# Optimization experiments

Hardware: AMD Instinct MI355X
Metric: run time of the kernel (lower is better)

## Reference

```python
import jax, jax.numpy as jnp
import numpy as np

HEADS, HEAD_DIM, NQP, NVP = 12, 16, 4, 8
NODE_DIM, EDGE_DIM = 384, 128
B, N = 1, 768


def setup_inputs() -> dict:
    key = jax.random.key(0)
    ks = jax.random.split(key, 12)
    node_features = jax.random.normal(ks[0], (B, N, NODE_DIM), dtype=jnp.float32)
    edge_features = jax.random.normal(ks[1], (B, N, N, EDGE_DIM), dtype=jnp.float32)
    # random valid rotations via QR of gaussian matrices (well-conditioned for inverse)
    A = jax.random.normal(ks[2], (B, N, 3, 3), dtype=jnp.float32)
    Q, _ = jnp.linalg.qr(A)
    R = Q
    t = jax.random.normal(ks[3], (B, N, 3), dtype=jnp.float32)
    def lin(k, din, dout):
        return jax.random.normal(k, (din, dout), dtype=jnp.float32) / np.sqrt(din)
    Wqkv = lin(ks[4], NODE_DIM, 3 * HEADS * HEAD_DIM)
    Wvqk = lin(ks[5], NODE_DIM, 2 * 3 * NQP * HEADS)
    Wvv = lin(ks[6], NODE_DIM, 3 * NVP * HEADS)
    Webias = lin(ks[7], EDGE_DIM, HEADS)
    fin_in = HEADS * EDGE_DIM + HEADS * HEAD_DIM + HEADS * NVP * 4
    Wfin = lin(ks[8], fin_in, NODE_DIM)
    bfin = jnp.zeros((NODE_DIM,), dtype=jnp.float32)
    return {"node_features": node_features, "edge_features": edge_features,
            "R": R, "t": t, "Wqkv": Wqkv, "Wvqk": Wvqk, "Wvv": Wvv,
            "Webias": Webias, "Wfin": Wfin, "bfin": bfin}


def _ipa(node_features, edge_features, R, t, Wqkv, Wvqk, Wvv, Webias, Wfin, bfin):
    b, n, _ = node_features.shape
    h, d, p, pv = HEADS, HEAD_DIM, NQP, NVP
    # scalar q, k, v: [b, h, n, d]
    qkv = (node_features @ Wqkv).reshape(b, n, 3, h, d)
    sq, sk, sv = [jnp.transpose(qkv[:, :, i], (0, 2, 1, 3)) for i in range(3)]
    node_scalar = jnp.einsum('bhid,bhjd->bhij', sq, sk) * (d ** -0.5)
    edge_bias = jnp.einsum('bijd,dh->bhij', edge_features, Webias)
    # vector q/k in local frames: [b, h, n, p, 3]
    vqk = (node_features @ Wvqk).reshape(b, n, 2, h, p, 3)
    vq = jnp.transpose(vqk[:, :, 0], (0, 2, 1, 3, 4))
    vk = jnp.transpose(vqk[:, :, 1], (0, 2, 1, 3, 4))
    t_e = t[:, None, :, None, :]  # [b,1,n,1,3]
    gq = jnp.einsum('bnij,bhnpj->bhnpi', R, vq) + t_e
    gk = jnp.einsum('bnij,bhnpj->bhnpi', R, vk) + t_e
    # ||gk_i - gq_j||^2 summed over (p,3), expanded to avoid [b,h,n,n,p,3]
    wc = np.sqrt(2.0 / 9.0 / p) / 2.0
    k_sq = jnp.sum(gk * gk, axis=(-1, -2))  # [b,h,n]
    q_sq = jnp.sum(gq * gq, axis=(-1, -2))  # [b,h,n]
    cross = jnp.einsum('bhipd,bhjpd->bhij', gk, gq)
    dist = (k_sq[:, :, :, None] + q_sq[:, :, None, :] - 2.0 * cross) * wc
    attn = jax.nn.softmax((node_scalar + edge_bias - dist) * (3 ** -0.5), axis=-1)
    # aggregations
    edge_out = jnp.einsum('bhij,bijd->bihd', attn, edge_features)     # [b,n,h,edge_dim]
    scalar_out = jnp.einsum('bhij,bhjd->bihd', attn, sv)              # [b,n,h,d]
    vv = (node_features @ Wvv).reshape(b, n, h, pv, 3)
    vv = jnp.transpose(vv, (0, 2, 1, 3, 4))                            # [b,h,n,pv,3]
    gvv = jnp.einsum('bnij,bhnpj->bhnpi', R, vv) + t_e
    att_v = jnp.einsum('bhij,bhjpd->bihpd', attn, gvv)                # [b,n,h,pv,3]
    Rinv = jnp.linalg.inv(R)
    local_v = jnp.einsum('bnij,bnhpj->bnhpi', Rinv, att_v - t[:, :, None, None, :])
    v_len = jnp.sqrt(jnp.sum(local_v * local_v, axis=-1))             # [b,n,h,pv]
    combined = jnp.concatenate([
        edge_out.reshape(b, n, -1),
        scalar_out.reshape(b, n, -1),
        local_v.reshape(b, n, -1),
        v_len.reshape(b, n, -1),
    ], axis=-1)
    return node_features + combined @ Wfin + bfin


def reference(node_features, edge_features, R, t, Wqkv, Wvqk, Wvv, Webias, Wfin, bfin):
    return _ipa(node_features, edge_features, R, t, Wqkv, Wvqk, Wvv, Webias, Wfin, bfin)
```

## Files before the change

### kernel.cpp

```cpp
#include <hip/hip_runtime.h>
#include <cmath>


namespace {

constexpr int NN = 768;
constexpr int NH = 12;

constexpr float S3 = 0.5773502691896258f;
constexpr float C1 = 0.25f * S3;
constexpr float C2 = 0.23570226039551584f * S3;
constexpr float C3 = 0.11785113019775792f * S3;

typedef float f32x4 __attribute__((ext_vector_type(4)));
typedef short bf16x8 __attribute__((ext_vector_type(8)));
typedef unsigned int u32x4 __attribute__((ext_vector_type(4)));
typedef unsigned int u32x2 __attribute__((ext_vector_type(2)));
typedef _Float16 f16x2 __attribute__((ext_vector_type(2)));

#define LGKM0 asm volatile("s_waitcnt lgkmcnt(0)" ::: "memory")
#define SCHED0 __builtin_amdgcn_sched_barrier(0)

__device__ inline unsigned cvt_pk_bf16(float lo, float hi) {
  unsigned r;
  asm volatile("v_cvt_pk_bf16_f32 %0, %1, %2" : "=v"(r) : "v"(lo), "v"(hi));
  return r;
}

__device__ inline float fdot2(unsigned a, unsigned b, float c) {
#if __has_builtin(__builtin_amdgcn_fdot2)
  return __builtin_amdgcn_fdot2(__builtin_bit_cast(f16x2, a),
                                __builtin_bit_cast(f16x2, b), c, false);
#else
  union U { unsigned u; _Float16 h[2]; } x, y;
  x.u = a; y.u = b;
  return c + (float)x.h[0] * (float)y.h[0] + (float)x.h[1] * (float)y.h[1];
#endif
}

__device__ inline u32x2 tr_read(unsigned addr) {
  u32x2 d;
  asm volatile("ds_read_b64_tr_b16 %0, %1" : "=v"(d) : "v"(addr));
  return d;
}

__device__ inline f32x4 mfma16(u32x2 a, u32x2 b, f32x4 c) {
  asm volatile("v_mfma_f32_16x16x16_bf16 %0, %1, %2, %0"
               : "+v"(c) : "v"(a), "v"(b));
  return c;
}

__device__ inline unsigned pkf16(float a, float b) {
  union U { _Float16 h[2]; unsigned u; } x;
  x.h[0] = (_Float16)a; x.h[1] = (_Float16)b;
  return x.u;
}

__global__ __launch_bounds__(288) void k_proj(const float* __restrict__ node,
    const float* __restrict__ Wqkv, const float* __restrict__ Wvqk,
    const float* __restrict__ Wvv, float* __restrict__ proj) {
  __shared__ __align__(16) float nl[2][384];
  const int i0 = blockIdx.x * 2;
  const int tid = threadIdx.x;
  for (int idx = tid; idx < 2 * 384; idx += 288)
    ((float*)nl)[idx] = node[(size_t)i0 * 384 + idx];
  __syncthreads();
  const int c0 = tid * 4;
  const float* W; int ld, col;
  if (c0 < 576)      { W = Wqkv; ld = 576; col = c0; }
  else if (c0 < 864) { W = Wvqk; ld = 288; col = c0 - 576; }
  else               { W = Wvv;  ld = 288; col = c0 - 864; }
  float4 acc[2];
#pragma unroll
  for (int r = 0; r < 2; ++r) acc[r] = make_float4(0.f, 0.f, 0.f, 0.f);
#pragma unroll 4
  for (int k = 0; k < 384; ++k) {
    const float4 w4 = *(const float4*)&W[(size_t)k * ld + col];
#pragma unroll
    for (int r = 0; r < 2; ++r) {
      const float nv = nl[r][k];
      acc[r].x += nv * w4.x; acc[r].y += nv * w4.y;
      acc[r].z += nv * w4.z; acc[r].w += nv * w4.w;
    }
  }
#pragma unroll
  for (int r = 0; r < 2; ++r)
    *(float4*)&proj[(size_t)(i0 + r) * 1152 + c0] = acc[r];
}

__global__ __launch_bounds__(256) void k_geom(const float* __restrict__ proj,
    const float* __restrict__ R, const float* __restrict__ t,
    unsigned* __restrict__ Bph, unsigned* __restrict__ Sgh,
    float* __restrict__ V) {
  const int gid = blockIdx.x * 256 + threadIdx.x;
  if (gid >= NN * NH) return;
  const int n = gid / NH, h = gid % NH;
  const float* pr = proj + (size_t)n * 1152;
  const float* Rn = R + n * 9;
  const float t0 = t[n * 3 + 0], t1 = t[n * 3 + 1], t2 = t[n * 3 + 2];
  const size_t hn = (size_t)h * NN + n;
  unsigned* bp = Bph + ((size_t)n * NH + h) * 16;
  unsigned* sg = Sgh + ((size_t)n * NH + h) * 16;
#pragma unroll
  for (int m = 0; m < 8; ++m) {
    bp[m] = pkf16(C1 * pr[(12 + h) * 16 + 2 * m], C1 * pr[(12 + h) * 16 + 2 * m + 1]);
    sg[m] = pkf16(pr[h * 16 + 2 * m], pr[h * 16 + 2 * m + 1]);
    V[hn * 40 + 2 * m]     = pr[(24 + h) * 16 + 2 * m];
    V[hn * 40 + 2 * m + 1] = pr[(24 + h) * 16 + 2 * m + 1];
  }
  float gq[12], gk[12];
  float qs = 0.f, ks = 0.f;
#pragma unroll
  for (int p = 0; p < 4; ++p) {
    {
      const float vx = pr[576 + (h * 4 + p) * 3 + 0];
      const float vy = pr[576 + (h * 4 + p) * 3 + 1];
      const float vz = pr[576 + (h * 4 + p) * 3 + 2];
      const float g0 = Rn[0] * vx + Rn[1] * vy + Rn[2] * vz + t0;
      const float g1 = Rn[3] * vx + Rn[4] * vy + Rn[5] * vz + t1;
      const float g2 = Rn[6] * vx + Rn[7] * vy + Rn[8] * vz + t2;
      gq[p * 3 + 0] = g0; gq[p * 3 + 1] = g1; gq[p * 3 + 2] = g2;
      qs += g0 * g0 + g1 * g1 + g2 * g2;
    }
    {
      const float vx = pr[576 + ((12 + h) * 4 + p) * 3 + 0];
      const float vy = pr[576 + ((12 + h) * 4 + p) * 3 + 1];
      const float vz = pr[576 + ((12 + h) * 4 + p) * 3 + 2];
      const float g0 = Rn[0] * vx + Rn[1] * vy + Rn[2] * vz + t0;
      const float g1 = Rn[3] * vx + Rn[4] * vy + Rn[5] * vz + t1;
      const float g2 = Rn[6] * vx + Rn[7] * vy + Rn[8] * vz + t2;
      gk[p * 3 + 0] = g0; gk[p * 3 + 1] = g1; gk[p * 3 + 2] = g2;
      ks += g0 * g0 + g1 * g1 + g2 * g2;
    }
  }
#pragma unroll
  for (int m = 0; m < 6; ++m) {
    bp[8 + m] = pkf16(C2 * gq[2 * m], C2 * gq[2 * m + 1]);
    sg[8 + m] = pkf16(gk[2 * m], gk[2 * m + 1]);
  }
  bp[14] = pkf16(-C3 * qs, 1.0f);
  sg[14] = pkf16(1.0f, -C3 * ks);
  bp[15] = 0u; sg[15] = 0u;
#pragma unroll
  for (int p = 0; p < 8; ++p) {
    const float vx = pr[864 + (h * 8 + p) * 3 + 0];
    const float vy = pr[864 + (h * 8 + p) * 3 + 1];
    const float vz = pr[864 + (h * 8 + p) * 3 + 2];
    V[hn * 40 + 16 + p * 3 + 0] = Rn[0] * vx + Rn[1] * vy + Rn[2] * vz + t0;
    V[hn * 40 + 16 + p * 3 + 1] = Rn[3] * vx + Rn[4] * vy + Rn[5] * vz + t1;
    V[hn * 40 + 16 + p * 3 + 2] = Rn[6] * vx + Rn[7] * vy + Rn[8] * vz + t2;
  }
}

__global__ __launch_bounds__(256, 3) void k_fused(
    const float* __restrict__ edge, const float* __restrict__ Webias,
    const unsigned* __restrict__ Bph, const unsigned* __restrict__ Sgh,
    unsigned* __restrict__ pTu, float* __restrict__ m_t,
    float* __restrict__ eout, float* __restrict__ msm,
    float* __restrict__ linv) {
  __shared__ __align__(16) unsigned short etS[4][2112];
  __shared__ __align__(16) float Osh[4][8][16][16];
  __shared__ float msh[4][16];
  __shared__ float lsh[4][16];
  const int i = blockIdx.x;
  const int tid = threadIdx.x;
  const int lane = tid & 63;
  const int w = __builtin_amdgcn_readfirstlane(tid >> 6);
  const int g = lane >> 4;
  const int c16 = lane & 15;
  const int hc = c16 < 12 ? c16 : 11;

  const unsigned etbase =
      (unsigned)(uintptr_t)(__attribute__((address_space(3))) unsigned short*)&etS[w][0];

  bf16x8 wbfrag[4];
#pragma unroll
  for (int kk = 0; kk < 4; ++kk) {
    union Pk { unsigned u[4]; bf16x8 v; } pk;
#pragma unroll
    for (int e2 = 0; e2 < 4; ++e2) {
      const int d = kk * 32 + g * 8 + 2 * e2;
      const float lo = (c16 < 12) ? S3 * Webias[d * 12 + c16] : 0.f;
      const float hi = (c16 < 12) ? S3 * Webias[(d + 1) * 12 + c16] : 0.f;
      pk.u[e2] = cvt_pk_bf16(lo, hi);
    }
    wbfrag[kk] = pk.v;
  }

  const unsigned* sgp = Sgh + ((size_t)i * NH + hc) * 16;
  const u32x4 sg0 = *(const u32x4*)(sgp + 0);
  const u32x4 sg1 = *(const u32x4*)(sgp + 4);
  const u32x4 sg2 = *(const u32x4*)(sgp + 8);
  const u32x4 sg3 = *(const u32x4*)(sgp + 12);

  float m = -3.0e38f;
  float lsum = 0.f;
  f32x4 acc[8];
#pragma unroll
  for (int dt = 0; dt < 8; ++dt) acc[dt] = (f32x4){0.f, 0.f, 0.f, 0.f};

  float4 ra[8];
  auto load8 = [&](int t) {
    const int jw = t * 64 + w * 16;
#pragma unroll
    for (int q = 0; q < 4; ++q) {
      const int f8 = lane + 64 * q;
      const int j = f8 >> 4, c8 = f8 & 15;
      const float* gp = &edge[((size_t)(i * NN + jw + j)) * 128 + c8 * 8];
      ra[2 * q]     = *(const float4*)gp;
      ra[2 * q + 1] = *(const float4*)(gp + 4);
    }
  };
  auto store8 = [&]() {
#pragma unroll
    for (int q = 0; q < 4; ++q) {
      const int f8 = lane + 64 * q;
      const int j = f8 >> 4, c8 = f8 & 15;
      u32x4 pk;
      pk.x = cvt_pk_bf16(ra[2 * q].x,     ra[2 * q].y);
      pk.y = cvt_pk_bf16(ra[2 * q].z,     ra[2 * q].w);
      pk.z = cvt_pk_bf16(ra[2 * q + 1].x, ra[2 * q + 1].y);
      pk.w = cvt_pk_bf16(ra[2 * q + 1].z, ra[2 * q + 1].w);
      *(u32x4*)&etS[w][(c8 >> 1) * 264 + j * 16 + 8 * (c8 & 1)] = pk;
    }
  };

  load8(0);

#pragma unroll 1
  for (int t = 0; t < 12; ++t) {
    const int tw = t * 4 + w;
    LGKM0;
    store8();
    SCHED0;
    if (t < 11) load8(t + 1);

    f32x4 ebacc = {0.f, 0.f, 0.f, 0.f};
#pragma unroll
    for (int kk = 0; kk < 4; ++kk) {
      const int dt = 2 * kk + (g >> 1);
      const bf16x8 a = *(const bf16x8*)&etS[w][dt * 264 + c16 * 16 + 8 * (g & 1)];
      ebacc = __builtin_amdgcn_mfma_f32_16x16x32_bf16(a, wbfrag[kk], ebacc, 0, 0, 0);
    }

    float lg[4];
#pragma unroll
    for (int r = 0; r < 4; ++r) {
      const unsigned* bpp = Bph + ((size_t)(tw * 16 + 4 * g + r) * NH + hc) * 16;
      const u32x4 b0 = *(const u32x4*)(bpp + 0);
      const u32x4 b1 = *(const u32x4*)(bpp + 4);
      const u32x4 b2 = *(const u32x4*)(bpp + 8);
      const u32x4 b3 = *(const u32x4*)(bpp + 12);
      float a = ebacc[r];
      a = fdot2(b0.x, sg0.x, a); a = fdot2(b0.y, sg0.y, a);
      a = fdot2(b0.z, sg0.z, a); a = fdot2(b0.w, sg0.w, a);
      a = fdot2(b1.x, sg1.x, a); a = fdot2(b1.y, sg1.y, a);
      a = fdot2(b1.z, sg1.z, a); a = fdot2(b1.w, sg1.w, a);
      a = fdot2(b2.x, sg2.x, a); a = fdot2(b2.y, sg2.y, a);
      a = fdot2(b2.z, sg2.z, a); a = fdot2(b2.w, sg2.w, a);
      a = fdot2(b3.x, sg3.x, a); a = fdot2(b3.y, sg3.y, a);
      a = fdot2(b3.z, sg3.z, a);
      lg[r] = a;
    }

    const float lmax = fmaxf(fmaxf(lg[0], lg[1]), fmaxf(lg[2], lg[3]));
    if (__any(lmax > m + 6.f)) {
      float tm = lmax;
      tm = fmaxf(tm, __shfl_xor(tm, 16, 64));
      tm = fmaxf(tm, __shfl_xor(tm, 32, 64));
      const float mn = fmaxf(m, tm);
      const float f = __expf(m - mn);
      m = mn;
      lsum *= f;
      float fr[4];
#pragma unroll
      for (int r = 0; r < 4; ++r) fr[r] = __shfl(f, 4 * g + r, 64);
#pragma unroll
      for (int dt = 0; dt < 8; ++dt) {
        acc[dt][0] *= fr[0]; acc[dt][1] *= fr[1];
        acc[dt][2] *= fr[2]; acc[dt][3] *= fr[3];
      }
    }
    float p0 = __expf(lg[0] - m), p1 = __expf(lg[1] - m);
    float p2 = __expf(lg[2] - m), p3 = __expf(lg[3] - m);
    lsum += (p0 + p1) + (p2 + p3);
    const unsigned pk0 = cvt_pk_bf16(p0, p1);
    const unsigned pk1 = cvt_pk_bf16(p2, p3);
    pTu[((size_t)i * 48 + tw) * 128 + g * 16 + c16]      = pk0;
    pTu[((size_t)i * 48 + tw) * 128 + 64 + g * 16 + c16] = pk1;
    if (g == 0) m_t[((size_t)i * 48 + tw) * 16 + c16] = m;

    u32x2 bfr[8];
#pragma unroll
    for (int dt = 0; dt < 8; ++dt) {
      const unsigned addr = etbase + (unsigned)(dt * 528 + g * 128 + c16 * 8);
      bfr[dt] = tr_read(addr);
    }
    LGKM0; SCHED0;
    u32x2 apk; apk.x = pk0; apk.y = pk1;
#pragma unroll
    for (int dt = 0; dt < 8; ++dt) acc[dt] = mfma16(apk, bfr[dt], acc[dt]);
  }

#pragma unroll
  for (int dt = 0; dt < 8; ++dt)
#pragma unroll
    for (int r = 0; r < 4; ++r)
      Osh[w][dt][c16][4 * g + r] = acc[dt][r];
  float ls = lsum;
  ls += __shfl_xor(ls, 16, 64);
  ls += __shfl_xor(ls, 32, 64);
  if (lane < 16) { msh[w][lane] = m; lsh[w][lane] = ls; }
  __syncthreads();
  for (int idx = tid; idx < 12 * 128; idx += 256) {
    const int h = idx >> 7, d = idx & 127;
    const int dt = d >> 4, dp = d & 15;
    const float m0 = msh[0][h], m1 = msh[1][h], m2 = msh[2][h], m3 = msh[3][h];
    const float mb = fmaxf(fmaxf(m0, m1), fmaxf(m2, m3));
    const float f0 = __expf(m0 - mb), f1 = __expf(m1 - mb);
    const float f2 = __expf(m2 - mb), f3 = __expf(m3 - mb);
    const float lb = lsh[0][h] * f0 + lsh[1][h] * f1 + lsh[2][h] * f2 + lsh[3][h] * f3;
    const float O = Osh[0][dt][dp][h] * f0 + Osh[1][dt][dp][h] * f1
                  + Osh[2][dt][dp][h] * f2 + Osh[3][dt][dp][h] * f3;
    eout[(size_t)i * 1536 + h * 128 + d] = O / lb;
    if (d == 0) {
      msm[(size_t)h * NN + i] = mb;
      linv[(size_t)h * NN + i] = 1.0f / lb;
    }
  }
}

__global__ __launch_bounds__(320) void k_scav(const unsigned* __restrict__ pTu,
    const float* __restrict__ m_t, const float* __restrict__ msm,
    const float* __restrict__ linv, const float* __restrict__ V,
    float* __restrict__ scav) {
  __shared__ __align__(16) float At[64][20];
  __shared__ __align__(16) float Vt[64][40];
  __shared__ __align__(16) float red[320 * 8];
  const int i0 = blockIdx.x * 16;
  const int h  = blockIdx.y;
  const int tid = threadIdx.x;
  const int js = tid / 80, rem = tid % 80;
  const int rg = rem / 20, cp = rem % 20;
  float2 a0 = {0.f, 0.f}, a1 = {0.f, 0.f}, a2 = {0.f, 0.f}, a3 = {0.f, 0.f};
  for (int jt = 0; jt < 12; ++jt) {
    __syncthreads();
    for (int idx = tid; idx < 1024; idx += 320) {
      const int r = idx >> 6, jj = idx & 63;
      const int i = i0 + r;
      const int tw = jt * 4 + (jj >> 4);
      const int gg = (jj & 15) >> 2, e = jj & 3;
      const unsigned u = pTu[((size_t)i * 48 + tw) * 128 + (e >> 1) * 64 + gg * 16 + h];
      const float p = __uint_as_float((e & 1) ? (u & 0xffff0000u) : (u << 16));
      const float fac = __expf(m_t[((size_t)i * 48 + tw) * 16 + h] - msm[(size_t)h * NN + i])
                      * linv[(size_t)h * NN + i];
      At[jj][r] = p * fac;
    }
    for (int idx = tid; idx < 2560; idx += 320) {
      const int jj = idx / 40, c = idx % 40;
      Vt[jj][c] = V[((size_t)h * NN + jt * 64 + jj) * 40 + c];
    }
    __syncthreads();
#pragma unroll 4
    for (int s = 0; s < 16; ++s) {
      const int jj = js * 16 + s;
      const float4 a4 = *(const float4*)&At[jj][rg * 4];
      const float2 b2 = *(const float2*)&Vt[jj][cp * 2];
      a0.x += a4.x * b2.x; a0.y += a4.x * b2.y;
      a1.x += a4.y * b2.x; a1.y += a4.y * b2.y;
      a2.x += a4.z * b2.x; a2.y += a4.z * b2.y;
      a3.x += a4.w * b2.x; a3.y += a4.w * b2.y;
    }
  }
  __syncthreads();
  *(float4*)&red[tid * 8 + 0] = make_float4(a0.x, a0.y, a1.x, a1.y);
  *(float4*)&red[tid * 8 + 4] = make_float4(a2.x, a2.y, a3.x, a3.y);
  __syncthreads();
  if (tid < 80) {
    const int rg2 = tid / 20, cp2 = tid % 20;
    float4 s0 = make_float4(0.f, 0.f, 0.f, 0.f), s1 = s0;
#pragma unroll
    for (int q = 0; q < 4; ++q) {
      const float4 r0 = *(const float4*)&red[(tid + q * 80) * 8 + 0];
      const float4 r1 = *(const float4*)&red[(tid + q * 80) * 8 + 4];
      s0.x += r0.x; s0.y += r0.y; s0.z += r0.z; s0.w += r0.w;
      s1.x += r1.x; s1.y += r1.y; s1.z += r1.z; s1.w += r1.w;
    }
    const size_t base = (size_t)h * NN + i0 + rg2 * 4;
    *(float2*)&scav[(base + 0) * 40 + cp2 * 2] = make_float2(s0.x, s0.y);
    *(float2*)&scav[(base + 1) * 40 + cp2 * 2] = make_float2(s0.z, s0.w);
    *(float2*)&scav[(base + 2) * 40 + cp2 * 2] = make_float2(s1.x, s1.y);
    *(float2*)&scav[(base + 3) * 40 + cp2 * 2] = make_float2(s1.z, s1.w);
  }
}

__global__ __launch_bounds__(256) void k_comb(
    const float* __restrict__ R, const float* __restrict__ t,
    const float* __restrict__ eout, const float* __restrict__ scav,
    float* __restrict__ comb) {
  const int i0 = blockIdx.x * 4;
  const int tid = threadIdx.x;
  __shared__ float rinv[4][9];
  __shared__ float tl[4][3];
  if (tid < 4) {
    const int i = i0 + tid;
    const float* Rn = R + i * 9;
    const float r00 = Rn[0], r01 = Rn[1], r02 = Rn[2];
    const float r10 = Rn[3], r11 = Rn[4], r12 = Rn[5];
    const float r20 = Rn[6], r21 = Rn[7], r22 = Rn[8];
    const float det = r00 * (r11 * r22 - r12 * r21)
                    - r01 * (r10 * r22 - r12 * r20)
                    + r02 * (r10 * r21 - r11 * r20);
    const float id = 1.0f / det;
    rinv[tid][0] = (r11 * r22 - r12 * r21) * id;
    rinv[tid][1] = (r02 * r21 - r01 * r22) * id;
    rinv[tid][2] = (r01 * r12 - r02 * r11) * id;
    rinv[tid][3] = (r12 * r20 - r10 * r22) * id;
    rinv[tid][4] = (r00 * r22 - r02 * r20) * id;
    rinv[tid][5] = (r02 * r10 - r00 * r12) * id;
    rinv[tid][6] = (r10 * r21 - r11 * r20) * id;
    rinv[tid][7] = (r01 * r20 - r00 * r21) * id;
    rinv[tid][8] = (r00 * r11 - r01 * r10) * id;
    tl[tid][0] = t[i * 3 + 0]; tl[tid][1] = t[i * 3 + 1]; tl[tid][2] = t[i * 3 + 2];
  }
  __syncthreads();
  for (int idx = tid; idx < 4 * 2112; idx += 256) {
    const int r = idx / 2112, k = idx % 2112;
    const int i = i0 + r;
    float val;
    if (k < 1536) {
      val = eout[(size_t)i * 1536 + k];
    } else if (k < 1728) {
      const int s = k - 1536, h = s >> 4, d = s & 15;
      val = scav[((size_t)h * NN + i) * 40 + d];
    } else if (k < 2016) {
      const int s = k - 1728, h = s / 24, rem = s % 24, p = rem / 3, x = rem % 3;
      const float* av = scav + ((size_t)h * NN + i) * 40 + 16 + p * 3;
      const float a0 = av[0] - tl[r][0], a1 = av[1] - tl[r][1], a2 = av[2] - tl[r][2];
      val = rinv[r][x * 3 + 0] * a0 + rinv[r][x * 3 + 1] * a1 + rinv[r][x * 3 + 2] * a2;
    } else {
      const int s = k - 2016, h = s >> 3, p = s & 7;
      const float* av = scav + ((size_t)h * NN + i) * 40 + 16 + p * 3;
      const float a0 = av[0] - tl[r][0], a1 = av[1] - tl[r][1], a2 = av[2] - tl[r][2];
      const float l0 = rinv[r][0] * a0 + rinv[r][1] * a1 + rinv[r][2] * a2;
      const float l1 = rinv[r][3] * a0 + rinv[r][4] * a1 + rinv[r][5] * a2;
      const float l2 = rinv[r][6] * a0 + rinv[r][7] * a1 + rinv[r][8] * a2;
      val = sqrtf(l0 * l0 + l1 * l1 + l2 * l2);
    }
    comb[(size_t)i * 2112 + k] = val;
  }
}

__global__ __launch_bounds__(256) void k_finalA(
    const float* __restrict__ comb, const float* __restrict__ Wfin,
    float* __restrict__ partial) {
  __shared__ __align__(16) float cl[64][36];
  __shared__ __align__(16) float wl[32][68];
  const int i0 = blockIdx.x * 64;
  const int c0 = blockIdx.y * 64;
  const int k0 = blockIdx.z * 192;
  const int tid = threadIdx.x;
  const int cq = tid & 15, rq = tid >> 4;
  float4 acc[4];
#pragma unroll
  for (int r = 0; r < 4; ++r) acc[r] = make_float4(0.f, 0.f, 0.f, 0.f);
  for (int sub = 0; sub < 6; ++sub) {
    const int kc = k0 + sub * 32;
    __syncthreads();
#pragma unroll
    for (int half = 0; half < 2; ++half) {
      const int qi = tid + half * 256;
      const int r = qi >> 3, kq = qi & 7;
      *(float4*)&cl[r][kq * 4] = *(const float4*)&comb[(size_t)(i0 + r) * 2112 + kc + kq * 4];
      const int kk = qi >> 4, cc = qi & 15;
      *(float4*)&wl[kk][cc * 4] = *(const float4*)&Wfin[(size_t)(kc + kk) * 384 + c0 + cc * 4];
    }
    __syncthreads();
#pragma unroll
    for (int k4 = 0; k4 < 8; ++k4) {
      float4 a[4], wv[4];
#pragma unroll
      for (int r = 0; r < 4; ++r) a[r] = *(const float4*)&cl[rq * 4 + r][k4 * 4];
#pragma unroll
      for (int q = 0; q < 4; ++q) wv[q] = *(const float4*)&wl[k4 * 4 + q][cq * 4];
#pragma unroll
      for (int r = 0; r < 4; ++r) {
        acc[r].x += a[r].x * wv[0].x + a[r].y * wv[1].x + a[r].z * wv[2].x + a[r].w * wv[3].x;
        acc[r].y += a[r].x * wv[0].y + a[r].y * wv[1].y + a[r].z * wv[2].y + a[r].w * wv[3].y;
        acc[r].z += a[r].x * wv[0].z + a[r].y * wv[1].z + a[r].z * wv[2].z + a[r].w * wv[3].z;
        acc[r].w += a[r].x * wv[0].w + a[r].y * wv[1].w + a[r].z * wv[2].w + a[r].w * wv[3].w;
      }
    }
  }
#pragma unroll
  for (int r = 0; r < 4; ++r)
    *(float4*)&partial[((size_t)blockIdx.z * NN + i0 + rq * 4 + r) * 384 + c0 + cq * 4] = acc[r];
}

__global__ __launch_bounds__(256) void k_finalB(const float* __restrict__ node,
    const float* __restrict__ partial, const float* __restrict__ bfin,
    float* __restrict__ out) {
  const int gid = blockIdx.x * 256 + threadIdx.x;
  const int i = gid / 96, cq = gid % 96;
  float4 v = *(const float4*)&node[(size_t)i * 384 + cq * 4];
  const float4 b = *(const float4*)&bfin[cq * 4];
  v.x += b.x; v.y += b.y; v.z += b.z; v.w += b.w;
#pragma unroll
  for (int s = 0; s < 11; ++s) {
    const float4 p = *(const float4*)&partial[((size_t)s * NN + i) * 384 + cq * 4];
    v.x += p.x; v.y += p.y; v.z += p.z; v.w += p.w;
  }
  *(float4*)&out[(size_t)i * 384 + cq * 4] = v;
}

}

extern "C" void kernel_launch(void* const* d_in, const int* in_sizes, int n_in,
                              void* d_out, int out_size, void* d_ws, size_t ws_size,
                              hipStream_t stream) {
  const float* node   = (const float*)d_in[0];
  const float* edge   = (const float*)d_in[1];
  const float* R      = (const float*)d_in[2];
  const float* t      = (const float*)d_in[3];
  const float* Wqkv   = (const float*)d_in[4];
  const float* Wvqk   = (const float*)d_in[5];
  const float* Wvv    = (const float*)d_in[6];
  const float* Webias = (const float*)d_in[7];
  const float* Wfin   = (const float*)d_in[8];
  const float* bfin   = (const float*)d_in[9];
  float* out = (float*)d_out;

  float* ws = (float*)d_ws;
  float*    proj = ws;
  float*    V    = proj + 884736;
  unsigned* Bph  = (unsigned*)(V + 368640);
  unsigned* Sgh  = Bph + 147456;
  unsigned* pTu  = Sgh + 147456;
  float*    m_t  = (float*)(pTu + 4718592);
  float*    eout = m_t + 589824;
  float*    scav = eout + 1179648;
  float*    msm  = scav + 368640;
  float*    linv = msm + 9216;
  float* comb    = (float*)pTu;
  float* partial = comb + 1622016;

  hipLaunchKernelGGL(k_proj, dim3(384), dim3(288), 0, stream,
                     node, Wqkv, Wvqk, Wvv, proj);
  hipLaunchKernelGGL(k_geom, dim3(36), dim3(256), 0, stream,
                     proj, R, t, Bph, Sgh, V);
  hipLaunchKernelGGL(k_fused, dim3(768), dim3(256), 0, stream,
                     edge, Webias, Bph, Sgh, pTu, m_t, eout, msm, linv);
  hipLaunchKernelGGL(k_scav, dim3(48, 12), dim3(320), 0, stream,
                     pTu, m_t, msm, linv, V, scav);
  hipLaunchKernelGGL(k_comb, dim3(192), dim3(256), 0, stream,
                     R, t, eout, scav, comb);
  hipLaunchKernelGGL(k_finalA, dim3(12, 6, 11), dim3(256), 0, stream,
                     comb, Wfin, partial);
  hipLaunchKernelGGL(k_finalB, dim3(288), dim3(256), 0, stream,
                     node, partial, bfin, out);
}
```

Baseline: 251.7 us.

## Cut k_fused register and LDS footprint to raise occupancy to four blocks

The bf16 Webias MFMA fragments are now precomputed once in k_geom into a small workspace buffer and reloaded per tile, and the Sgh row is reloaded inside the loop rather than held in registers. The transposed LDS reads and MFMAs are split into two halves of four, so fewer B fragments are live at once. The partial output tile is stored as bf16 in the same per-wave LDS region as the edge tile, and launch bounds rise from 3 to 4 blocks per CU. The trade is extra global/cache loads per tile and an added bf16 rounding of the partial sums before the cross-wave softmax merge.

```diff
diff --git a/kernel.cpp b/kernel.cpp
--- a/kernel.cpp
+++ b/kernel.cpp
@@ -90,9 +90,24 @@
 
 __global__ __launch_bounds__(256) void k_geom(const float* __restrict__ proj,
     const float* __restrict__ R, const float* __restrict__ t,
+    const float* __restrict__ Webias,
     unsigned* __restrict__ Bph, unsigned* __restrict__ Sgh,
-    float* __restrict__ V) {
+    float* __restrict__ V, unsigned* __restrict__ WbP) {
   const int gid = blockIdx.x * 256 + threadIdx.x;
+  if (blockIdx.x == 0) {
+    const int tid = threadIdx.x;
+    const int lane = tid & 63, kk = tid >> 6;
+    const int colB = lane & 15, gB = lane >> 4;
+    u32x4 wv;
+#pragma unroll
+    for (int e = 0; e < 4; ++e) {
+      const int d = kk * 32 + gB * 8 + 2 * e;
+      const float lo = (colB < 12) ? S3 * Webias[d * 12 + colB] : 0.f;
+      const float hi = (colB < 12) ? S3 * Webias[(d + 1) * 12 + colB] : 0.f;
+      wv[e] = cvt_pk_bf16(lo, hi);
+    }
+    *(u32x4*)&WbP[(size_t)tid * 4] = wv;
+  }
   if (gid >= NN * NH) return;
   const int n = gid / NH, h = gid % NH;
   const float* pr = proj + (size_t)n * 1152;
@@ -152,16 +167,13 @@
   }
 }
 
-__global__ __launch_bounds__(256, 3) void k_fused(
-    const float* __restrict__ edge, const float* __restrict__ Webias,
+__global__ __launch_bounds__(256, 4) void k_fused(
+    const float* __restrict__ edge, const unsigned* __restrict__ WbP,
     const unsigned* __restrict__ Bph, const unsigned* __restrict__ Sgh,
     unsigned* __restrict__ pTu, float* __restrict__ m_t,
     float* __restrict__ eout, float* __restrict__ msm,
     float* __restrict__ linv) {
-  __shared__ __align__(16) unsigned short etS[4][2112];
-  __shared__ __align__(16) float Osh[4][8][16][16];
-  __shared__ float msh[4][16];
-  __shared__ float lsh[4][16];
+  __shared__ __align__(16) unsigned char wreg[4][4224];
   const int i = blockIdx.x;
   const int tid = threadIdx.x;
   const int lane = tid & 63;
@@ -170,28 +182,9 @@
   const int c16 = lane & 15;
   const int hc = c16 < 12 ? c16 : 11;
 
+  unsigned short* etSw = (unsigned short*)&wreg[w][0];
   const unsigned etbase =
-      (unsigned)(uintptr_t)(__attribute__((address_space(3))) unsigned short*)&etS[w][0];
-
-  bf16x8 wbfrag[4];
-#pragma unroll
-  for (int kk = 0; kk < 4; ++kk) {
-    union Pk { unsigned u[4]; bf16x8 v; } pk;
-#pragma unroll
-    for (int e2 = 0; e2 < 4; ++e2) {
-      const int d = kk * 32 + g * 8 + 2 * e2;
-      const float lo = (c16 < 12) ? S3 * Webias[d * 12 + c16] : 0.f;
-      const float hi = (c16 < 12) ? S3 * Webias[(d + 1) * 12 + c16] : 0.f;
-      pk.u[e2] = cvt_pk_bf16(lo, hi);
-    }
-    wbfrag[kk] = pk.v;
-  }
-
-  const unsigned* sgp = Sgh + ((size_t)i * NH + hc) * 16;
-  const u32x4 sg0 = *(const u32x4*)(sgp + 0);
-  const u32x4 sg1 = *(const u32x4*)(sgp + 4);
-  const u32x4 sg2 = *(const u32x4*)(sgp + 8);
-  const u32x4 sg3 = *(const u32x4*)(sgp + 12);
+      (unsigned)(uintptr_t)(__attribute__((address_space(3))) unsigned char*)&wreg[w][0];
 
   float m = -3.0e38f;
   float lsum = 0.f;
@@ -221,7 +214,7 @@
       pk.y = cvt_pk_bf16(ra[2 * q].z,     ra[2 * q].w);
       pk.z = cvt_pk_bf16(ra[2 * q + 1].x, ra[2 * q + 1].y);
       pk.w = cvt_pk_bf16(ra[2 * q + 1].z, ra[2 * q + 1].w);
-      *(u32x4*)&etS[w][(c8 >> 1) * 264 + j * 16 + 8 * (c8 & 1)] = pk;
+      *(u32x4*)&etSw[(c8 >> 1) * 264 + j * 16 + 8 * (c8 & 1)] = pk;
     }
   };
 
@@ -239,10 +232,17 @@
 #pragma unroll
     for (int kk = 0; kk < 4; ++kk) {
       const int dt = 2 * kk + (g >> 1);
-      const bf16x8 a = *(const bf16x8*)&etS[w][dt * 264 + c16 * 16 + 8 * (g & 1)];
-      ebacc = __builtin_amdgcn_mfma_f32_16x16x32_bf16(a, wbfrag[kk], ebacc, 0, 0, 0);
-    }
-
+      const bf16x8 a = *(const bf16x8*)&etSw[dt * 264 + c16 * 16 + 8 * (g & 1)];
+      const u32x4 wv = *(const u32x4*)&WbP[(size_t)(kk * 64 + lane) * 4];
+      const bf16x8 b = __builtin_bit_cast(bf16x8, wv);
+      ebacc = __builtin_amdgcn_mfma_f32_16x16x32_bf16(a, b, ebacc, 0, 0, 0);
+    }
+
+    const unsigned* sgp = Sgh + ((size_t)i * NH + hc) * 16;
+    const u32x4 sg0 = *(const u32x4*)(sgp + 0);
+    const u32x4 sg1 = *(const u32x4*)(sgp + 4);
+    const u32x4 sg2 = *(const u32x4*)(sgp + 8);
+    const u32x4 sg3 = *(const u32x4*)(sgp + 12);
     float lg[4];
 #pragma unroll
     for (int r = 0; r < 4; ++r) {
@@ -290,38 +290,55 @@
     pTu[((size_t)i * 48 + tw) * 128 + 64 + g * 16 + c16] = pk1;
     if (g == 0) m_t[((size_t)i * 48 + tw) * 16 + c16] = m;
 
-    u32x2 bfr[8];
+    u32x2 apk; apk.x = pk0; apk.y = pk1;
+    u32x2 bfr[4];
+#pragma unroll
+    for (int half = 0; half < 2; ++half) {
+#pragma unroll
+      for (int q = 0; q < 4; ++q)
+        bfr[q] = tr_read(etbase + (unsigned)((half * 4 + q) * 528 + g * 128 + c16 * 8));
+      LGKM0; SCHED0;
+#pragma unroll
+      for (int q = 0; q < 4; ++q)
+        acc[half * 4 + q] = mfma16(apk, bfr[q], acc[half * 4 + q]);
+    }
+  }
+
+  {
+    unsigned short* OshW = (unsigned short*)&wreg[w][0];
 #pragma unroll
     for (int dt = 0; dt < 8; ++dt) {
-      const unsigned addr = etbase + (unsigned)(dt * 528 + g * 128 + c16 * 8);
-      bfr[dt] = tr_read(addr);
-    }
-    LGKM0; SCHED0;
-    u32x2 apk; apk.x = pk0; apk.y = pk1;
-#pragma unroll
-    for (int dt = 0; dt < 8; ++dt) acc[dt] = mfma16(apk, bfr[dt], acc[dt]);
-  }
-
-#pragma unroll
-  for (int dt = 0; dt < 8; ++dt)
-#pragma unroll
-    for (int r = 0; r < 4; ++r)
-      Osh[w][dt][c16][4 * g + r] = acc[dt][r];
-  float ls = lsum;
-  ls += __shfl_xor(ls, 16, 64);
-  ls += __shfl_xor(ls, 32, 64);
-  if (lane < 16) { msh[w][lane] = m; lsh[w][lane] = ls; }
+      u32x2 pkk;
+      pkk.x = cvt_pk_bf16(acc[dt][0], acc[dt][1]);
+      pkk.y = cvt_pk_bf16(acc[dt][2], acc[dt][3]);
+      *(u32x2*)&OshW[dt * 256 + c16 * 16 + g * 4] = pkk;
+    }
+    float ls = lsum;
+    ls += __shfl_xor(ls, 16, 64);
+    ls += __shfl_xor(ls, 32, 64);
+    if (lane < 16) {
+      *(float*)&wreg[w][4096 + lane * 4] = m;
+      *(float*)&wreg[w][4160 + lane * 4] = ls;
+    }
+  }
   __syncthreads();
   for (int idx = tid; idx < 12 * 128; idx += 256) {
     const int h = idx >> 7, d = idx & 127;
     const int dt = d >> 4, dp = d & 15;
-    const float m0 = msh[0][h], m1 = msh[1][h], m2 = msh[2][h], m3 = msh[3][h];
-    const float mb = fmaxf(fmaxf(m0, m1), fmaxf(m2, m3));
-    const float f0 = __expf(m0 - mb), f1 = __expf(m1 - mb);
-    const float f2 = __expf(m2 - mb), f3 = __expf(m3 - mb);
-    const float lb = lsh[0][h] * f0 + lsh[1][h] * f1 + lsh[2][h] * f2 + lsh[3][h] * f3;
-    const float O = Osh[0][dt][dp][h] * f0 + Osh[1][dt][dp][h] * f1
-                  + Osh[2][dt][dp][h] * f2 + Osh[3][dt][dp][h] * f3;
+    float mv[4], lv[4], Ov[4];
+#pragma unroll
+    for (int w2 = 0; w2 < 4; ++w2) {
+      mv[w2] = *(const float*)&wreg[w2][4096 + h * 4];
+      lv[w2] = *(const float*)&wreg[w2][4160 + h * 4];
+      const unsigned short us =
+          *(const unsigned short*)&wreg[w2][(dt * 256 + dp * 16 + h) * 2];
+      Ov[w2] = __uint_as_float(((unsigned)us) << 16);
+    }
+    const float mb = fmaxf(fmaxf(mv[0], mv[1]), fmaxf(mv[2], mv[3]));
+    const float f0 = __expf(mv[0] - mb), f1 = __expf(mv[1] - mb);
+    const float f2 = __expf(mv[2] - mb), f3 = __expf(mv[3] - mb);
+    const float lb = lv[0] * f0 + lv[1] * f1 + lv[2] * f2 + lv[3] * f3;
+    const float O = Ov[0] * f0 + Ov[1] * f1 + Ov[2] * f2 + Ov[3] * f3;
     eout[(size_t)i * 1536 + h * 128 + d] = O / lb;
     if (d == 0) {
       msm[(size_t)h * NN + i] = mb;
@@ -535,7 +552,8 @@
   float*    V    = proj + 884736;
   unsigned* Bph  = (unsigned*)(V + 368640);
   unsigned* Sgh  = Bph + 147456;
-  unsigned* pTu  = Sgh + 147456;
+  unsigned* WbP  = Sgh + 147456;
+  unsigned* pTu  = WbP + 1024;
   float*    m_t  = (float*)(pTu + 4718592);
   float*    eout = m_t + 589824;
   float*    scav = eout + 1179648;
@@ -547,9 +565,9 @@
   hipLaunchKernelGGL(k_proj, dim3(384), dim3(288), 0, stream,
                      node, Wqkv, Wvqk, Wvv, proj);
   hipLaunchKernelGGL(k_geom, dim3(36), dim3(256), 0, stream,
-                     proj, R, t, Bph, Sgh, V);
+                     proj, R, t, Webias, Bph, Sgh, V, WbP);
   hipLaunchKernelGGL(k_fused, dim3(768), dim3(256), 0, stream,
-                     edge, Webias, Bph, Sgh, pTu, m_t, eout, msm, linv);
+                     edge, WbP, Bph, Sgh, pTu, m_t, eout, msm, linv);
   hipLaunchKernelGGL(k_scav, dim3(48, 12), dim3(320), 0, stream,
                      pTu, m_t, msm, linv, V, scav);
   hipLaunchKernelGGL(k_comb, dim3(192), dim3(256), 0, stream,
```

Result: no change. 256.1 us (+1.7%).
